# Performance work log

Hardware: AMD Instinct MI355X
Metric: run time of the kernel (lower is better)

## Reference

```python
import jax, jax.numpy as jnp
import numpy as np

LMAX = 3                               # self.lmax = lmax_arg(2) + 1
L2 = LMAX * LMAX                       # 9 = 1 + 3 + 5
N_MLP = 2
DEG_IDX = np.repeat(np.arange(LMAX), 2 * np.arange(LMAX) + 1)   # [9] block -> degree index
SEG = np.zeros((LMAX, L2), np.float32)                          # one-hot segment matrix [3,9]
SEG[DEG_IDX, np.arange(L2)] = 1.0


def setup_inputs() -> dict:
    key = jax.random.key(0)
    ks = jax.random.split(key, 8)
    B, M, F, K = 8, 1024, 64, 64
    x = jax.random.normal(ks[0], (B, M, F, L2), jnp.float32)
    y = jax.random.normal(ks[1], (B, M, F, L2), jnp.float32)
    # Glorot-ish scales so tanh stays in its active range
    s0 = 1.0 / np.sqrt(F * F * LMAX)
    sh = 1.0 / np.sqrt(K)
    wx0 = jax.random.normal(ks[2], (K, F, F, LMAX), jnp.float32) * s0
    wy0 = jax.random.normal(ks[3], (K, F, F, LMAX), jnp.float32) * s0
    wx_h = jax.random.normal(ks[4], (N_MLP, K, K), jnp.float32) * sh
    wy_h = jax.random.normal(ks[5], (N_MLP, K, K), jnp.float32) * sh
    wxf = jax.random.normal(ks[6], (LMAX, F, K), jnp.float32) * sh
    wyf = jax.random.normal(ks[7], (LMAX, F, K), jnp.float32) * sh
    return {"x": x, "y": y, "wx0": wx0, "wy0": wy0,
            "wx_h": wx_h, "wy_h": wy_h, "wxf": wxf, "wyf": wyf}


def reference(x, y, wx0, wy0, wx_h, wy_h, wxf, wyf):
    seg = jnp.asarray(SEG)                                   # [lmax, l2]
    # cross-product gate from the l=1 (vector) components
    x1 = x[..., 1:4]                                         # [B,M,F,3]
    y1 = y[..., 1:4]
    gate = jnp.sum(jnp.cross(x1, y1) * y[..., 0:3], axis=-1) # [B,M,F]
    xg = x * gate[..., None]                                 # gated x, [B,M,F,l2]
    # outer product over features + contiguous segment-sum over degree blocks
    # mix[b,m,f,g,l] = sum_{s in block l} xg[b,m,g,s] * y[b,m,f,s]
    mix = jnp.einsum('bmgs,bmfs,ls->bmfgl', xg, y, seg)      # [B,M,F,F,lmax]
    mix_x = jnp.einsum('bmfgl,kfgl->bmk', mix, wx0)          # [B,M,k]
    mix_y = jnp.einsum('bmfgl,kfgl->bmk', mix, wy0)
    for i in range(N_MLP):
        mix_x = jnp.tanh(mix_x @ wx_h[i])
        mix_y = jnp.tanh(mix_y @ wy_h[i])
    mix_x = jnp.tanh(jnp.einsum('bmk,lfk->bmfl', mix_x, wxf))  # [B,M,F,lmax]
    mix_y = jnp.tanh(jnp.einsum('bmk,lfk->bmfl', mix_y, wyf))
    # broadcast each degree back over its 2l+1 components (gather == tf.repeat)
    res = mix_x[..., DEG_IDX] * xg + mix_y[..., DEG_IDX] * y   # [B,M,F,l2]
    return res
```

## Files before the change

### kernel.cpp

```cpp
#include <hip/hip_runtime.h>
#include <hip/hip_bf16.h>

typedef __attribute__((ext_vector_type(8))) short short8;
typedef __attribute__((ext_vector_type(16))) float f32x16;
typedef __fp16 h2 __attribute__((ext_vector_type(2)));
typedef unsigned short ushort_t;

#define DEVFN static __device__ __forceinline__
#define MFMA32 __builtin_amdgcn_mfma_f32_32x32x16_bf16

DEVFN float bf2f(unsigned short u){
  union { unsigned int i; float f; } v; v.i = ((unsigned int)u) << 16; return v.f;
}
DEVFN unsigned short f2bf(float f){
  unsigned int u = __float_as_uint(f);
  unsigned int r = u + 0x7FFFu + ((u >> 16) & 1u);
  return (unsigned short)(r >> 16);
}
DEVFN unsigned int pkbf(float a, float b){
  unsigned int r;
  asm("v_cvt_pk_bf16_f32 %0, %1, %2" : "=v"(r) : "v"(a), "v"(b));
  return r;
}
DEVFN h2 pkrtz(float a, float b){ return __builtin_amdgcn_cvt_pkrtz(a, b); }
DEVFN h2 u2h(unsigned int u){ union { unsigned int u; h2 h; } v; v.u = u; return v.h; }
#if __has_builtin(__builtin_amdgcn_fdot2)
DEVFN float fdot2(h2 a, h2 b, float c){ return __builtin_amdgcn_fdot2(a, b, c, false); }
#else
DEVFN float fdot2(h2 a, h2 b, float c){ return c + (float)a[0]*(float)b[0] + (float)a[1]*(float)b[1]; }
#endif
DEVFN float tanh_fast(float x){
  float t = __builtin_amdgcn_exp2f(x * 2.885390081777926815f);
  return 1.0f - 2.0f * __builtin_amdgcn_rcpf(t + 1.0f);
}
DEVFN int kmap(int h, int j){ return 4*h + (j & 3) + 8*(j >> 2); }

__global__ void bake_w0(const float* __restrict__ wx0, const float* __restrict__ wy0,
                        ushort_t* __restrict__ wfrag){
  int idx = blockIdx.x * 256 + threadIdx.x;
  int g = idx & 63; int r = idx >> 6;
  int f = r & 63; r >>= 6;
  int k = r & 63; int path = r >> 6;
  const float* w = path ? wy0 : wx0;
  const float* src = w + ((size_t)(k*64 + f)*64 + g)*3;
  float v0 = src[0], v1 = src[1], v2 = src[2];
  int gq = g >> 4, gl = g & 15;
  int h = (gl >> 2) & 1;
  int j = (gl & 3) | ((gl >> 3) << 2);
  int lane = h*32 + (k & 31);
  int nt = k >> 5;
  size_t base = (size_t)((f*4 + gq)*2 + path)*3072 + (size_t)lane*8 + j;
  wfrag[base + 0*512 + (size_t)nt*512] = f2bf(v0);
  wfrag[base + 2*512 + (size_t)nt*512] = f2bf(v1);
  wfrag[base + 4*512 + (size_t)nt*512] = f2bf(v2);
}

__global__ void bake_wh(const float* __restrict__ wxh, const float* __restrict__ wyh,
                        ushort_t* __restrict__ whfrag){
  int slot = blockIdx.x * 256 + threadIdx.x;
  int lane = slot & 63;
  int q = slot >> 6;
  int nt = q & 1; q >>= 1;
  int c  = q & 3; q >>= 2;
  int path = q & 1; int layer = q >> 1;
  const float* w = path ? wyh : wxh;
  int n = nt*32 + (lane & 31);
  int h = lane >> 5;
  unsigned int pk[4];
#pragma unroll
  for (int jj = 0; jj < 4; ++jj){
    int k0 = c*16 + kmap(h, 2*jj);
    int k1 = c*16 + kmap(h, 2*jj + 1);
    unsigned int b0 = f2bf(w[layer*4096 + k0*64 + n]);
    unsigned int b1 = f2bf(w[layer*4096 + k1*64 + n]);
    pk[jj] = b0 | (b1 << 16);
  }
  *reinterpret_cast<uint4*>(whfrag + (size_t)slot * 8) = make_uint4(pk[0], pk[1], pk[2], pk[3]);
}

__global__ void bake_wf(const float* __restrict__ wxf, const float* __restrict__ wyf,
                        ushort_t* __restrict__ wffrag){
  int slot = blockIdx.x * 256 + threadIdx.x;
  int lane = slot & 63;
  int q = slot >> 6;
  int ntf = q % 6;
  int q2 = q / 6;
  int c = q2 & 3; int path = q2 >> 2;
  const float* w = path ? wyf : wxf;
  int n = ntf*32 + (lane & 31);
  int lw = n >> 6, fw = n & 63;
  int h = lane >> 5;
  unsigned int pk[4];
#pragma unroll
  for (int jj = 0; jj < 4; ++jj){
    int k0 = c*16 + kmap(h, 2*jj);
    int k1 = c*16 + kmap(h, 2*jj + 1);
    unsigned int b0 = f2bf(w[(lw*64 + fw)*64 + k0]);
    unsigned int b1 = f2bf(w[(lw*64 + fw)*64 + k1]);
    pk[jj] = b0 | (b1 << 16);
  }
  *reinterpret_cast<uint4*>(wffrag + (size_t)slot * 8) = make_uint4(pk[0], pk[1], pk[2], pk[3]);
}

struct BSet { uint4 b[6]; };
union U4 { uint4 u; short8 s; };

__global__ __launch_bounds__(256)
void gemm10(const float* __restrict__ x, const float* __restrict__ y,
            const ushort_t* __restrict__ wfrag, float* __restrict__ mix){
  extern __shared__ char lds[];
  unsigned int* YHd = (unsigned int*)lds;
  ushort_t* YHh = (ushort_t*)lds;
  float (*red)[33] = (float (*)[33])(lds + 41600);

  const int bid = blockIdx.x;
  const int id = (bid & 7)*64 + (bid >> 3);
  const int nh = id & 1, mb = id >> 1;
  const int pbase = mb * 32;

  const int t = threadIdx.x, lane = t & 63, gq = t >> 6;
  const int h = lane >> 5, pr = lane & 31;

  const float* yb = y + (size_t)pbase * 576;

#pragma unroll
  for (int c = 0; c < 18; ++c){
    int q = t + c*256;
    int p = q / 144, off = (q - p*144) * 4;
    float4 v = *(const float4*)(yb + p*576 + off);
#pragma unroll
    for (int i = 0; i < 4; ++i){
      int flat = off + i;
      int f = flat / 9, s = flat - f*9;
      float vv = (i==0) ? v.x : (i==1) ? v.y : (i==2) ? v.z : v.w;
      union { __fp16 hf; ushort_t u; } cv; cv.hf = (__fp16)vv;
      YHh[p*650 + f*10 + s] = cv.u;
    }
  }
  __syncthreads();

  h2 xg[8][5];
#pragma unroll
  for (int j = 0; j < 8; ++j){
    const int g = gq*16 + kmap(h, j);
    const float* xp = x + (size_t)(pbase + pr)*576 + g*9;
    unsigned int yd0 = YHd[pr*325 + g*5 + 0];
    unsigned int yd1 = YHd[pr*325 + g*5 + 1];
    h2 y01 = u2h(yd0), y23v = u2h(yd1);
    float y0 = (float)y01[0], y1 = (float)y01[1];
    float y2 = (float)y23v[0], y3 = (float)y23v[1];
    float x1 = xp[1], x2 = xp[2], x3 = xp[3];
    float gate = (x2*y3 - x3*y2)*y0 + (x3*y1 - x1*y3)*y1 + (x1*y2 - x2*y1)*y2;
    xg[j][0] = pkrtz(xp[0]*gate, x1*gate);
    xg[j][1] = pkrtz(x2*gate, x3*gate);
    xg[j][2] = pkrtz(xp[4]*gate, xp[5]*gate);
    xg[j][3] = pkrtz(xp[6]*gate, xp[7]*gate);
    xg[j][4] = pkrtz(xp[8]*gate, 0.f);
  }

  f32x16 acc0, acc1;
#pragma unroll
  for (int e = 0; e < 16; ++e){ acc0[e] = 0.f; acc1[e] = 0.f; }

  const ushort_t* wt = wfrag + (size_t)(gq*2 + nh)*3072 + (size_t)lane*8;
  const unsigned int* yrow = YHd + pr*325;

  auto ldB = [&](int f, BSet& B){
    const ushort_t* p0 = wt + (size_t)f * 24576;
#pragma unroll
    for (int i = 0; i < 6; ++i) B.b[i] = *reinterpret_cast<const uint4*>(p0 + i*512);
  };
  auto ldYh = [&](int f, unsigned int* Yr){
#pragma unroll
    for (int d = 0; d < 5; ++d) Yr[d] = yrow[f*5 + d];
  };
  auto agen_mfma = [&](const unsigned int* Yr, const BSet& B){
    h2 y0m = u2h(Yr[0] & 0xFFFFu);
    h2 y1m = u2h(Yr[0] & 0xFFFF0000u);
    h2 y23 = u2h(Yr[1]), y45 = u2h(Yr[2]), y67 = u2h(Yr[3]);
    h2 y8p = u2h(Yr[4] & 0xFFFFu);
    float a0[8], a1[8], a2[8];
#pragma unroll
    for (int j = 0; j < 8; ++j){
      a0[j] = fdot2(xg[j][0], y0m, 0.f);
      a1[j] = fdot2(xg[j][1], y23, fdot2(xg[j][0], y1m, 0.f));
      a2[j] = fdot2(xg[j][4], y8p, fdot2(xg[j][3], y67, fdot2(xg[j][2], y45, 0.f)));
    }
    U4 fA0, fA1, fA2;
    fA0.u = make_uint4(pkbf(a0[0],a0[1]), pkbf(a0[2],a0[3]), pkbf(a0[4],a0[5]), pkbf(a0[6],a0[7]));
    fA1.u = make_uint4(pkbf(a1[0],a1[1]), pkbf(a1[2],a1[3]), pkbf(a1[4],a1[5]), pkbf(a1[6],a1[7]));
    fA2.u = make_uint4(pkbf(a2[0],a2[1]), pkbf(a2[2],a2[3]), pkbf(a2[4],a2[5]), pkbf(a2[6],a2[7]));
    U4 b0, b1, b2, b3, b4, b5;
    b0.u = B.b[0]; b1.u = B.b[1]; b2.u = B.b[2];
    b3.u = B.b[3]; b4.u = B.b[4]; b5.u = B.b[5];
    acc0 = MFMA32(fA0.s, b0.s, acc0, 0, 0, 0);
    acc1 = MFMA32(fA0.s, b1.s, acc1, 0, 0, 0);
    acc0 = MFMA32(fA1.s, b2.s, acc0, 0, 0, 0);
    acc1 = MFMA32(fA1.s, b3.s, acc1, 0, 0, 0);
    acc0 = MFMA32(fA2.s, b4.s, acc0, 0, 0, 0);
    acc1 = MFMA32(fA2.s, b5.s, acc1, 0, 0, 0);
  };

  BSet Ba, Bb;
  unsigned int Ya[5], Yb[5];
  ldB(0, Ba); ldYh(0, Ya);
  ldB(1, Bb); ldYh(1, Yb);

#pragma unroll 1
  for (int s = 0; s < 64; s += 2){
    agen_mfma(Ya, Ba);
    const int s2 = (s + 2 < 64) ? s + 2 : 63;
    ldB(s2, Ba); ldYh(s2, Ya);
    agen_mfma(Yb, Bb);
    const int s3 = (s + 3 < 64) ? s + 3 : 63;
    ldB(s3, Bb); ldYh(s3, Yb);
  }

  __syncthreads();
#pragma unroll 1
  for (int rr = 1; rr <= 3; ++rr){
    if (gq == rr){
#pragma unroll
      for (int e = 0; e < 16; ++e){
        red[lane][e]      = acc0[e];
        red[lane][16 + e] = acc1[e];
      }
    }
    __syncthreads();
    if (gq == 0){
#pragma unroll
      for (int e = 0; e < 16; ++e){
        acc0[e] += red[lane][e];
        acc1[e] += red[lane][16 + e];
      }
    }
    __syncthreads();
  }
  if (gq == 0){
#pragma unroll
    for (int e = 0; e < 16; ++e){
      int rowm = (e & 3) + 8*(e >> 2) + 4*h;
      float* d = mix + (size_t)(pbase + rowm)*128 + nh*64 + pr;
      d[0]  = acc0[e];
      d[32] = acc1[e];
    }
  }
}

__global__ __launch_bounds__(256, 1)
void mlp_core(const ushort_t* __restrict__ whfrag,
              const ushort_t* __restrict__ wffrag,
              const float* __restrict__ mix,
              ushort_t* __restrict__ oxg, ushort_t* __restrict__ oyg){
  extern __shared__ char ldsm[];
  ushort_t* hw = (ushort_t*)ldsm;
  const int t = threadIdx.x;
  const long pbase = (long)blockIdx.x * 32;

  {
    int p = t >> 3, n0 = (t & 7) * 16;
    const float* src = mix + (pbase + p)*128 + n0;
    int path = n0 >> 6, nn = n0 & 63;
    ushort_t* dst = hw + (path*2)*2176 + p*68 + nn;
#pragma unroll
    for (int q2 = 0; q2 < 16; ++q2) dst[q2] = f2bf(src[q2]);
  }
  __syncthreads();

  const int w = t >> 6, lane = t & 63;
  const int path = w >> 1, ntw = w & 1;
  const int prow = lane & 31, h = lane >> 5;
  int cur = 0;

#pragma unroll
  for (int layer = 0; layer < 2; ++layer){
    const ushort_t* act = hw + (path*2 + cur)*2176;
    f32x16 acc;
#pragma unroll
    for (int r = 0; r < 16; ++r) acc[r] = 0.f;
#pragma unroll
    for (int c = 0; c < 4; ++c){
      int ab = prow*68 + c*16 + 4*h;
      ushort4 lo = *(const ushort4*)&act[ab];
      ushort4 hi = *(const ushort4*)&act[ab + 8];
      short8 av; av[0]=lo.x; av[1]=lo.y; av[2]=lo.z; av[3]=lo.w;
      av[4]=hi.x; av[5]=hi.y; av[6]=hi.z; av[7]=hi.w;
      short8 bv = *(const short8*)(whfrag + ((((layer*2 + path)*4 + c)*2 + ntw)*512 + lane*8));
      acc = MFMA32(av, bv, acc, 0, 0, 0);
    }
    ushort_t* nact = hw + (path*2 + (cur ^ 1))*2176;
#pragma unroll
    for (int r = 0; r < 16; ++r){
      int p = (r & 3) + 8*(r >> 2) + 4*h;
      nact[p*68 + ntw*32 + prow] = f2bf(tanh_fast(acc[r]));
    }
    cur ^= 1;
    __syncthreads();
  }

  {
    const ushort_t* act = hw + (path*2 + cur)*2176;
    ushort_t* og = (path ? oyg : oxg) + (size_t)pbase * 196;
#pragma unroll
    for (int e = 0; e < 3; ++e){
      int ntf = ntw*3 + e;
      f32x16 acc;
#pragma unroll
      for (int r = 0; r < 16; ++r) acc[r] = 0.f;
#pragma unroll
      for (int c = 0; c < 4; ++c){
        int ab = prow*68 + c*16 + 4*h;
        ushort4 lo = *(const ushort4*)&act[ab];
        ushort4 hi = *(const ushort4*)&act[ab + 8];
        short8 av; av[0]=lo.x; av[1]=lo.y; av[2]=lo.z; av[3]=lo.w;
        av[4]=hi.x; av[5]=hi.y; av[6]=hi.z; av[7]=hi.w;
        short8 bv = *(const short8*)(wffrag + (((path*4 + c)*6 + ntf)*512 + lane*8));
        acc = MFMA32(av, bv, acc, 0, 0, 0);
      }
#pragma unroll
      for (int r = 0; r < 16; ++r){
        int p = (r & 3) + 8*(r >> 2) + 4*h;
        og[(size_t)p*196 + ntf*32 + prow] = f2bf(tanh_fast(acc[r]));
      }
    }
  }
}

__global__ __launch_bounds__(256)
void epilogue_k(const float* __restrict__ x, const float* __restrict__ y,
                const ushort_t* __restrict__ oxg, const ushort_t* __restrict__ oyg,
                float* __restrict__ out){
  __shared__ float xs[2304], ys[2304], os[2304];
  const int t = threadIdx.x;
  const long pbase = (long)blockIdx.x * 4;
  const float4* xb = (const float4*)(x + pbase*576);
  const float4* yb = (const float4*)(y + pbase*576);
#pragma unroll
  for (int c = 0; c < 3; ++c){
    int q = t + c*256;
    if (q < 576){
      ((float4*)xs)[q] = xb[q];
      ((float4*)ys)[q] = yb[q];
    }
  }
  __syncthreads();

  const int pp = t >> 6, fq = t & 63;
  {
    const float* xr = &xs[pp*576 + fq*9];
    const float* yr = &ys[pp*576 + fq*9];
    float xv[9], yv[9];
#pragma unroll
    for (int s = 0; s < 9; ++s){ xv[s] = xr[s]; yv[s] = yr[s]; }
    float c0 = xv[2]*yv[3] - xv[3]*yv[2];
    float c1 = xv[3]*yv[1] - xv[1]*yv[3];
    float c2 = xv[1]*yv[2] - xv[2]*yv[1];
    float gate = c0*yv[0] + c1*yv[1] + c2*yv[2];
    const size_t prow = (size_t)(pbase + pp) * 196;
    float ox0 = bf2f(oxg[prow + fq]);
    float ox1 = bf2f(oxg[prow + 64 + fq]);
    float ox2 = bf2f(oxg[prow + 128 + fq]);
    float oy0 = bf2f(oyg[prow + fq]);
    float oy1 = bf2f(oyg[prow + 64 + fq]);
    float oy2 = bf2f(oyg[prow + 128 + fq]);
    float* orow = &os[pp*576 + fq*9];
    orow[0] = ox0*xv[0]*gate + oy0*yv[0];
#pragma unroll
    for (int s = 1; s < 4; ++s) orow[s] = ox1*xv[s]*gate + oy1*yv[s];
#pragma unroll
    for (int s = 4; s < 9; ++s) orow[s] = ox2*xv[s]*gate + oy2*yv[s];
  }
  __syncthreads();

  float4* ob = (float4*)(out + pbase*576);
#pragma unroll
  for (int c = 0; c < 3; ++c){
    int q = t + c*256;
    if (q < 576) ob[q] = ((const float4*)os)[q];
  }
}

extern "C" void kernel_launch(void* const* d_in, const int* in_sizes, int n_in,
                              void* d_out, int out_size, void* d_ws, size_t ws_size,
                              hipStream_t stream){
  (void)in_sizes; (void)n_in; (void)out_size; (void)ws_size;
  const float* x   = (const float*)d_in[0];
  const float* y   = (const float*)d_in[1];
  const float* wx0 = (const float*)d_in[2];
  const float* wy0 = (const float*)d_in[3];
  const float* wxh = (const float*)d_in[4];
  const float* wyh = (const float*)d_in[5];
  const float* wxf = (const float*)d_in[6];
  const float* wyf = (const float*)d_in[7];
  float* out = (float*)d_out;
  char* ws = (char*)d_ws;
  ushort_t* wfrag  = (ushort_t*)(ws);
  ushort_t* whfrag = (ushort_t*)(ws + 3145728);
  ushort_t* wffrag = (ushort_t*)(ws + 3178496);
  float* mix       = (float*)(ws + 3227648);
  ushort_t* oxg    = (ushort_t*)(ws + 7421952);
  ushort_t* oyg    = (ushort_t*)(ws + 10633216);

  (void)hipFuncSetAttribute((const void*)gemm10,
        hipFuncAttributeMaxDynamicSharedMemorySize, 50048);

  hipLaunchKernelGGL(bake_w0, dim3(2048), dim3(256), 0, stream, wx0, wy0, wfrag);
  hipLaunchKernelGGL(bake_wh, dim3(8),    dim3(256), 0, stream, wxh, wyh, whfrag);
  hipLaunchKernelGGL(bake_wf, dim3(12),   dim3(256), 0, stream, wxf, wyf, wffrag);
  hipLaunchKernelGGL(gemm10,  dim3(512),  dim3(256), 50048, stream, x, y, wfrag, mix);
  hipLaunchKernelGGL(mlp_core, dim3(256), dim3(256), 17408, stream, whfrag, wffrag, mix, oxg, oyg);
  hipLaunchKernelGGL(epilogue_k, dim3(2048), dim3(256), 0, stream, x, y, oxg, oyg, out);
}
```

Baseline: 86.05 us.

## Split gemm reduction over f into two halves and stage x through LDS

The main gemm kernel now splits the f (reduction) dimension into two halves across separate blocks, doubling the grid to 1024 blocks. Each block writes a partial mix buffer, and mlp_core adds the two partials when loading. x is also staged through LDS as fp16 with coalesced loads instead of strided per-lane global reads, and the LDS footprint shrinks because only half of y is staged for the main loop. This adds parallelism and occupancy for a grid that previously had few waves per CU. The cost is an extra partial-sum buffer write and read, redundant gate computation in both halves, and x now rounded to fp16 before gating.

```diff
diff --git a/kernel.cpp b/kernel.cpp
--- a/kernel.cpp
+++ b/kernel.cpp
@@ -106,21 +106,22 @@
 union U4 { uint4 u; short8 s; };
 
 __global__ __launch_bounds__(256)
-void gemm10(const float* __restrict__ x, const float* __restrict__ y,
-            const ushort_t* __restrict__ wfrag, float* __restrict__ mix){
+void gemm14(const float* __restrict__ x, const float* __restrict__ y,
+            const ushort_t* __restrict__ wfrag, float* __restrict__ mixp){
   extern __shared__ char lds[];
-  unsigned int* YHd = (unsigned int*)lds;
-  ushort_t* YHh = (ushort_t*)lds;
-  float (*red)[33] = (float (*)[33])(lds + 41600);
+  unsigned int* Ld = (unsigned int*)lds;
+  ushort_t* Lh = (ushort_t*)lds;
+  float (*red)[33] = (float (*)[33])(lds + 21120);
 
   const int bid = blockIdx.x;
-  const int id = (bid & 7)*64 + (bid >> 3);
-  const int nh = id & 1, mb = id >> 1;
+  const int id = (bid & 7)*128 + (bid >> 3);
+  const int fh = id & 1, nh = (id >> 1) & 1, mb = id >> 2;
   const int pbase = mb * 32;
 
   const int t = threadIdx.x, lane = t & 63, gq = t >> 6;
   const int h = lane >> 5, pr = lane & 31;
 
+  const float* xb = x + (size_t)pbase * 576;
   const float* yb = y + (size_t)pbase * 576;
 
 #pragma unroll
@@ -134,36 +135,86 @@
       int f = flat / 9, s = flat - f*9;
       float vv = (i==0) ? v.x : (i==1) ? v.y : (i==2) ? v.z : v.w;
       union { __fp16 hf; ushort_t u; } cv; cv.hf = (__fp16)vv;
-      YHh[p*650 + f*10 + s] = cv.u;
-    }
-  }
-  __syncthreads();
-
-  h2 xg[8][5];
+      Lh[p*640 + f*10 + s] = cv.u;
+    }
+  }
+  __syncthreads();
+
+  float gy[8][4];
+  int gidx[8];
 #pragma unroll
   for (int j = 0; j < 8; ++j){
     const int g = gq*16 + kmap(h, j);
-    const float* xp = x + (size_t)(pbase + pr)*576 + g*9;
-    unsigned int yd0 = YHd[pr*325 + g*5 + 0];
-    unsigned int yd1 = YHd[pr*325 + g*5 + 1];
-    h2 y01 = u2h(yd0), y23v = u2h(yd1);
-    float y0 = (float)y01[0], y1 = (float)y01[1];
-    float y2 = (float)y23v[0], y3 = (float)y23v[1];
-    float x1 = xp[1], x2 = xp[2], x3 = xp[3];
+    gidx[j] = g;
+    unsigned int d0 = Ld[pr*320 + g*5 + 0];
+    unsigned int d1 = Ld[pr*320 + g*5 + 1];
+    h2 y01 = u2h(d0), y23 = u2h(d1);
+    gy[j][0] = (float)y01[0]; gy[j][1] = (float)y01[1];
+    gy[j][2] = (float)y23[0]; gy[j][3] = (float)y23[1];
+  }
+  __syncthreads();
+
+#pragma unroll
+  for (int c = 0; c < 18; ++c){
+    int q = t + c*256;
+    int p = q / 144, off = (q - p*144) * 4;
+    float4 v = *(const float4*)(xb + p*576 + off);
+#pragma unroll
+    for (int i = 0; i < 4; ++i){
+      int flat = off + i;
+      int f = flat / 9, s = flat - f*9;
+      float vv = (i==0) ? v.x : (i==1) ? v.y : (i==2) ? v.z : v.w;
+      union { __fp16 hf; ushort_t u; } cv; cv.hf = (__fp16)vv;
+      Lh[p*640 + f*10 + s] = cv.u;
+    }
+  }
+  __syncthreads();
+
+  h2 xg[8][5];
+#pragma unroll
+  for (int j = 0; j < 8; ++j){
+    const int g = gidx[j];
+    unsigned int d0 = Ld[pr*320 + g*5 + 0];
+    unsigned int d1 = Ld[pr*320 + g*5 + 1];
+    unsigned int d2 = Ld[pr*320 + g*5 + 2];
+    unsigned int d3 = Ld[pr*320 + g*5 + 3];
+    unsigned int d4 = Ld[pr*320 + g*5 + 4];
+    h2 x01 = u2h(d0), x23 = u2h(d1), x45 = u2h(d2), x67 = u2h(d3), x8p = u2h(d4);
+    float x0 = (float)x01[0], x1 = (float)x01[1];
+    float x2 = (float)x23[0], x3 = (float)x23[1];
+    float y0 = gy[j][0], y1 = gy[j][1], y2 = gy[j][2], y3 = gy[j][3];
     float gate = (x2*y3 - x3*y2)*y0 + (x3*y1 - x1*y3)*y1 + (x1*y2 - x2*y1)*y2;
-    xg[j][0] = pkrtz(xp[0]*gate, x1*gate);
+    xg[j][0] = pkrtz(x0*gate, x1*gate);
     xg[j][1] = pkrtz(x2*gate, x3*gate);
-    xg[j][2] = pkrtz(xp[4]*gate, xp[5]*gate);
-    xg[j][3] = pkrtz(xp[6]*gate, xp[7]*gate);
-    xg[j][4] = pkrtz(xp[8]*gate, 0.f);
-  }
+    xg[j][2] = pkrtz((float)x45[0]*gate, (float)x45[1]*gate);
+    xg[j][3] = pkrtz((float)x67[0]*gate, (float)x67[1]*gate);
+    xg[j][4] = pkrtz((float)x8p[0]*gate, 0.f);
+  }
+  __syncthreads();
+
+#pragma unroll
+  for (int c = 0; c < 9; ++c){
+    int q = t + c*256;
+    int p = q / 72, off = (q - p*72) * 4;
+    float4 v = *(const float4*)(yb + p*576 + fh*288 + off);
+#pragma unroll
+    for (int i = 0; i < 4; ++i){
+      int flat = off + i;
+      int f = flat / 9, s = flat - f*9;
+      float vv = (i==0) ? v.x : (i==1) ? v.y : (i==2) ? v.z : v.w;
+      union { __fp16 hf; ushort_t u; } cv; cv.hf = (__fp16)vv;
+      Lh[p*330 + f*10 + s] = cv.u;
+    }
+  }
+  __syncthreads();
 
   f32x16 acc0, acc1;
 #pragma unroll
   for (int e = 0; e < 16; ++e){ acc0[e] = 0.f; acc1[e] = 0.f; }
 
-  const ushort_t* wt = wfrag + (size_t)(gq*2 + nh)*3072 + (size_t)lane*8;
-  const unsigned int* yrow = YHd + pr*325;
+  const ushort_t* wt = wfrag + (size_t)(fh*32)*24576
+                             + (size_t)(gq*2 + nh)*3072 + (size_t)lane*8;
+  const unsigned int* yrow = Ld + pr*165;
 
   auto ldB = [&](int f, BSet& B){
     const ushort_t* p0 = wt + (size_t)f * 24576;
@@ -207,12 +258,12 @@
   ldB(1, Bb); ldYh(1, Yb);
 
 #pragma unroll 1
-  for (int s = 0; s < 64; s += 2){
+  for (int s = 0; s < 32; s += 2){
     agen_mfma(Ya, Ba);
-    const int s2 = (s + 2 < 64) ? s + 2 : 63;
+    const int s2 = (s + 2 < 32) ? s + 2 : 31;
     ldB(s2, Ba); ldYh(s2, Ya);
     agen_mfma(Yb, Bb);
-    const int s3 = (s + 3 < 64) ? s + 3 : 63;
+    const int s3 = (s + 3 < 32) ? s + 3 : 31;
     ldB(s3, Bb); ldYh(s3, Yb);
   }
 
@@ -237,10 +288,11 @@
     __syncthreads();
   }
   if (gq == 0){
+    float* mp = mixp + (size_t)fh * 1048576;
 #pragma unroll
     for (int e = 0; e < 16; ++e){
       int rowm = (e & 3) + 8*(e >> 2) + 4*h;
-      float* d = mix + (size_t)(pbase + rowm)*128 + nh*64 + pr;
+      float* d = mp + (size_t)(pbase + rowm)*128 + nh*64 + pr;
       d[0]  = acc0[e];
       d[32] = acc1[e];
     }
@@ -250,7 +302,7 @@
 __global__ __launch_bounds__(256, 1)
 void mlp_core(const ushort_t* __restrict__ whfrag,
               const ushort_t* __restrict__ wffrag,
-              const float* __restrict__ mix,
+              const float* __restrict__ mixp,
               ushort_t* __restrict__ oxg, ushort_t* __restrict__ oyg){
   extern __shared__ char ldsm[];
   ushort_t* hw = (ushort_t*)ldsm;
@@ -259,11 +311,14 @@
 
   {
     int p = t >> 3, n0 = (t & 7) * 16;
-    const float* src = mix + (pbase + p)*128 + n0;
+    const float* src = mixp + (pbase + p)*128 + n0;
     int path = n0 >> 6, nn = n0 & 63;
     ushort_t* dst = hw + (path*2)*2176 + p*68 + nn;
 #pragma unroll
-    for (int q2 = 0; q2 < 16; ++q2) dst[q2] = f2bf(src[q2]);
+    for (int q2 = 0; q2 < 16; ++q2){
+      float v = src[q2] + src[q2 + 1048576];
+      dst[q2] = f2bf(v);
+    }
   }
   __syncthreads();
 
@@ -397,17 +452,17 @@
   ushort_t* wfrag  = (ushort_t*)(ws);
   ushort_t* whfrag = (ushort_t*)(ws + 3145728);
   ushort_t* wffrag = (ushort_t*)(ws + 3178496);
-  float* mix       = (float*)(ws + 3227648);
-  ushort_t* oxg    = (ushort_t*)(ws + 7421952);
-  ushort_t* oyg    = (ushort_t*)(ws + 10633216);
-
-  (void)hipFuncSetAttribute((const void*)gemm10,
-        hipFuncAttributeMaxDynamicSharedMemorySize, 50048);
+  float* mixp      = (float*)(ws + 3227648);
+  ushort_t* oxg    = (ushort_t*)(ws + 11616256);
+  ushort_t* oyg    = (ushort_t*)(ws + 14827520);
+
+  (void)hipFuncSetAttribute((const void*)gemm14,
+        hipFuncAttributeMaxDynamicSharedMemorySize, 40960);
 
   hipLaunchKernelGGL(bake_w0, dim3(2048), dim3(256), 0, stream, wx0, wy0, wfrag);
   hipLaunchKernelGGL(bake_wh, dim3(8),    dim3(256), 0, stream, wxh, wyh, whfrag);
   hipLaunchKernelGGL(bake_wf, dim3(12),   dim3(256), 0, stream, wxf, wyf, wffrag);
-  hipLaunchKernelGGL(gemm10,  dim3(512),  dim3(256), 50048, stream, x, y, wfrag, mix);
-  hipLaunchKernelGGL(mlp_core, dim3(256), dim3(256), 17408, stream, whfrag, wffrag, mix, oxg, oyg);
+  hipLaunchKernelGGL(gemm14,  dim3(1024), dim3(256), 40960, stream, x, y, wfrag, mixp);
+  hipLaunchKernelGGL(mlp_core, dim3(256), dim3(256), 17408, stream, whfrag, wffrag, mixp, oxg, oyg);
   hipLaunchKernelGGL(epilogue_k, dim3(2048), dim3(256), 0, stream, x, y, oxg, oyg, out);
 }
```

Measured after the change: 105.8 us. +23.0%, slower.
